# Kernel tuning notes

Hardware: AMD Instinct MI355X
Metric: run time of the kernel (lower is better)

## Reference

```python
import jax, jax.numpy as jnp
import numpy as np

B, C, L, OUT = 64, 256, 4096, 256
EPS = 1e-5


def setup_inputs() -> dict:
    key = jax.random.key(0)
    ks = jax.random.split(key, 8)
    s = 1.0 / np.sqrt(C)
    return {
        "x": jax.random.normal(ks[0], (B, C, L), dtype=jnp.float32),
        "Wq": jax.random.normal(ks[1], (C, C), dtype=jnp.float32) * s,
        "Wk": jax.random.normal(ks[2], (C, C), dtype=jnp.float32) * s,
        "Wv": jax.random.normal(ks[3], (C, C), dtype=jnp.float32) * s,
        "Wc": jax.random.normal(ks[4], (C, C), dtype=jnp.float32) * s,
        "Wout": jax.random.normal(ks[5], (OUT, C), dtype=jnp.float32) * s,
        "gamma": jnp.ones((C,), dtype=jnp.float32),
        "beta": jnp.zeros((C,), dtype=jnp.float32),
    }


def _conv1x1(W, x):
    # 1x1 Conv1d, no bias: (O,C) x (B,C,L) -> (B,O,L)
    return jnp.einsum("oc,bcl->bol", W, x)


def reference(x, Wq, Wk, Wv, Wc, Wout, gamma, beta):
    q = _conv1x1(Wq, x)  # (B,C,L)
    k = _conv1x1(Wk, x)  # (B,C,L)
    v = _conv1x1(Wv, x)  # (B,C,L)
    # batch-wise attention: att[b,d,l] = sum_c q[b,c,l]*k[d,c,l] / sqrt(C)
    att = jnp.einsum("bcl,dcl->bdl", q, k) / jnp.sqrt(jnp.asarray(C, x.dtype))
    att = jax.nn.softmax(att, axis=1)  # softmax over the key-batch axis
    # virt[b,c,l] = sum_d att[b,d,l] * v[d,c,l]
    virt = jnp.einsum("bdl,dcl->bcl", att, v)
    # GroupNorm(1, C): normalize over (C,L) per sample, per-channel affine
    mean = jnp.mean(virt, axis=(1, 2), keepdims=True)
    var = jnp.var(virt, axis=(1, 2), keepdims=True)
    virt = (virt - mean) * jax.lax.rsqrt(var + EPS)
    virt = virt * gamma[None, :, None] + beta[None, :, None]
    virt = jax.nn.relu(virt)
    virt = _conv1x1(Wc, virt)
    # dropout is identity in eval mode
    y = x + virt
    return _conv1x1(Wout, y)
```

## Files before the change

kernel.cpp:

```cpp
#include <hip/hip_runtime.h>


typedef __attribute__((ext_vector_type(8))) short          v8s;
typedef __attribute__((ext_vector_type(8))) unsigned short v8u;
typedef __attribute__((ext_vector_type(4))) unsigned short v4u;
typedef __attribute__((ext_vector_type(4))) float          f32x4;

#define MFMA16(a, b, c) __builtin_amdgcn_mfma_f32_16x16x32_bf16((a), (b), (c), 0, 0, 0)

#define GLOAD16(g, l)                                                            \
  __builtin_amdgcn_global_load_lds(                                              \
      (const __attribute__((address_space(1))) unsigned int*)(const void*)(g),   \
      (__attribute__((address_space(3))) unsigned int*)(void*)(l), 16, 0, 0)

static __device__ __forceinline__ unsigned short f2bf(float f) {
  union { float f; unsigned u; } v; v.f = f;
  unsigned r = (v.u + 0x7FFFu + ((v.u >> 16) & 1u)) >> 16;
  return (unsigned short)r;
}
static __device__ __forceinline__ float bf2f(unsigned short h) {
  union { unsigned u; float f; } v; v.u = ((unsigned)h) << 16; return v.f;
}

__global__ void k_prep(const float* __restrict__ Wq, const float* __restrict__ Wk,
                       const float* __restrict__ Wv, const float* __restrict__ Wc,
                       const float* __restrict__ Wout,
                       unsigned short* __restrict__ Wtv,
                       unsigned short* __restrict__ Wout2,
                       float* __restrict__ stats) {
  int bid = blockIdx.x, j = threadIdx.x;
  if (bid < 256) {
    int i = bid;
    float acc = 0.f;
    for (int c = 0; c < 256; ++c) acc += Wq[c * 256 + i] * Wk[c * 256 + j];
    Wtv[i * 256 + j] = f2bf(acc * 0.0625f);
    Wtv[(256 + i) * 256 + j] = f2bf(Wv[i * 256 + j]);
  } else if (bid < 512) {
    int o = bid - 256;
    float acc = 0.f;
    for (int c = 0; c < 256; ++c) acc += Wout[o * 256 + c] * Wc[c * 256 + j];
    Wout2[o * 512 + 256 + j] = f2bf(acc);
    Wout2[o * 512 + j] = f2bf(Wout[o * 256 + j]);
  } else {
    stats[(bid - 512) * 256 + j] = 0.f;
  }
}

__global__ void k_transpose(const float* __restrict__ x, unsigned short* __restrict__ Xt) {
  __shared__ float tile[64 * 65];
  int bid = blockIdx.x;
  int b = bid >> 8, cb = (bid >> 6) & 3, lb = bid & 63;
  int c0 = cb * 64, l0 = lb * 64, t = threadIdx.x;
#pragma unroll
  for (int i = 0; i < 4; ++i) {
    int idx = i * 256 + t, r = idx >> 4, ch = idx & 15;
    float4 v = *(const float4*)(x + ((size_t)(b * 256 + c0 + r)) * 4096 + l0 + ch * 4);
    tile[r * 65 + ch * 4 + 0] = v.x; tile[r * 65 + ch * 4 + 1] = v.y;
    tile[r * 65 + ch * 4 + 2] = v.z; tile[r * 65 + ch * 4 + 3] = v.w;
  }
  __syncthreads();
#pragma unroll
  for (int i = 0; i < 2; ++i) {
    int idx = i * 256 + t, r = idx >> 3, ch = idx & 7;
    v8u o;
#pragma unroll
    for (int j = 0; j < 8; ++j) o[j] = f2bf(tile[(ch * 8 + j) * 65 + r]);
    *(v8u*)(Xt + ((size_t)(b * 4096 + l0 + r)) * 256 + c0 + ch * 8) = o;
  }
}

__global__ __launch_bounds__(512, 4) void k_fused(const unsigned short* __restrict__ Xt,
                                                  const unsigned short* __restrict__ Wtv,
                                                  unsigned short* __restrict__ Virt,
                                                  float* __restrict__ stats) {
  extern __shared__ char smem[];
  unsigned short* Xs  = (unsigned short*)(smem);
  unsigned short* Tb  = (unsigned short*)(smem + 33792);
  unsigned short* Ps  = (unsigned short*)(smem + 70656);
  float*          red = (float*)(smem + 79872);
  float*          rowv= (float*)(smem + 80896);

  int l = blockIdx.x, t = threadIdx.x, lane = t & 63, w = t >> 6;
  int fr = lane & 15, kq = (lane >> 4) * 8, qr = (lane >> 4) * 4;

#pragma unroll
  for (int i = 0; i < 4; ++i) {
    int idx = i * 512 + t, r = idx >> 5, ch = idx & 31;
    *(v8u*)(Xs + r * 264 + ch * 8) = *(const v8u*)(Xt + ((size_t)(r * 4096 + l)) * 256 + ch * 8);
  }
  __syncthreads();

  {
    int n0 = w * 32;
    f32x4 acc[4][2];
#pragma unroll
    for (int mi = 0; mi < 4; ++mi)
#pragma unroll
      for (int nj = 0; nj < 2; ++nj) acc[mi][nj] = (f32x4){0.f, 0.f, 0.f, 0.f};
#pragma unroll
    for (int kc = 0; kc < 8; ++kc) {
      v8s a[4], b[2];
#pragma unroll
      for (int mi = 0; mi < 4; ++mi) a[mi] = *(const v8s*)(Xs + (mi * 16 + fr) * 264 + kc * 32 + kq);
#pragma unroll
      for (int nj = 0; nj < 2; ++nj)
        b[nj] = *(const v8s*)(Wtv + ((size_t)(n0 + nj * 16 + fr)) * 256 + kc * 32 + kq);
#pragma unroll
      for (int mi = 0; mi < 4; ++mi)
#pragma unroll
        for (int nj = 0; nj < 2; ++nj) acc[mi][nj] = MFMA16(a[mi], b[nj], acc[mi][nj]);
    }
#pragma unroll
    for (int mi = 0; mi < 4; ++mi)
#pragma unroll
      for (int nj = 0; nj < 2; ++nj)
#pragma unroll
        for (int i = 0; i < 4; ++i)
          Tb[(mi * 16 + qr + i) * 264 + n0 + nj * 16 + fr] = f2bf(acc[mi][nj][i]);
  }
  __syncthreads();

  int b0 = (w & 3) * 16, dp = (w >> 2) * 2, half = w >> 2;
  f32x4 sacc[2];
  sacc[0] = (f32x4){0.f, 0.f, 0.f, 0.f};
  sacc[1] = (f32x4){0.f, 0.f, 0.f, 0.f};
  {
#pragma unroll
    for (int kc = 0; kc < 8; ++kc) {
      v8s bb = *(const v8s*)(Xs + (b0 + fr) * 264 + kc * 32 + kq);
#pragma unroll
      for (int j = 0; j < 2; ++j) {
        v8s a = *(const v8s*)(Tb + ((dp + j) * 16 + fr) * 264 + kc * 32 + kq);
        sacc[j] = MFMA16(a, bb, sacc[j]);
      }
    }
    float pm = -1e30f;
#pragma unroll
    for (int j = 0; j < 2; ++j)
#pragma unroll
      for (int i = 0; i < 4; ++i) pm = fmaxf(pm, sacc[j][i]);
    pm = fmaxf(pm, __shfl_xor(pm, 16));
    pm = fmaxf(pm, __shfl_xor(pm, 32));
    if (lane < 16) red[(b0 + lane) * 4 + half] = pm;
  }
  __syncthreads();

  {
    float m = fmaxf(red[(b0 + fr) * 4 + 0], red[(b0 + fr) * 4 + 1]);
    float ps = 0.f;
#pragma unroll
    for (int j = 0; j < 2; ++j) {
      v4u pk;
#pragma unroll
      for (int i = 0; i < 4; ++i) {
        float e = __expf(sacc[j][i] - m);
        ps += e;
        pk[i] = f2bf(e);
      }
      *(v4u*)(Ps + (b0 + fr) * 72 + (dp + j) * 16 + qr) = pk;
    }
    ps += __shfl_xor(ps, 16);
    ps += __shfl_xor(ps, 32);
    if (lane < 16) red[(b0 + lane) * 4 + 2 + half] = ps;
  }

  {
    int c0 = w * 32;
    f32x4 vacc[2][4];
#pragma unroll
    for (int ci = 0; ci < 2; ++ci)
#pragma unroll
      for (int di = 0; di < 4; ++di) vacc[ci][di] = (f32x4){0.f, 0.f, 0.f, 0.f};
#pragma unroll
    for (int kc = 0; kc < 8; ++kc) {
      v8s a[2], b[4];
#pragma unroll
      for (int ci = 0; ci < 2; ++ci)
        a[ci] = *(const v8s*)(Wtv + ((size_t)(256 + c0 + ci * 16 + fr)) * 256 + kc * 32 + kq);
#pragma unroll
      for (int di = 0; di < 4; ++di) b[di] = *(const v8s*)(Xs + (di * 16 + fr) * 264 + kc * 32 + kq);
#pragma unroll
      for (int ci = 0; ci < 2; ++ci)
#pragma unroll
        for (int di = 0; di < 4; ++di) vacc[ci][di] = MFMA16(a[ci], b[di], vacc[ci][di]);
    }
#pragma unroll
    for (int ci = 0; ci < 2; ++ci)
#pragma unroll
      for (int di = 0; di < 4; ++di)
#pragma unroll
        for (int i = 0; i < 4; ++i)
          Tb[(c0 + ci * 16 + qr + i) * 72 + di * 16 + fr] = f2bf(vacc[ci][di][i]);
  }
  __syncthreads();

  if (t < 64) rowv[t] = 1.f / (red[t * 4 + 2] + red[t * 4 + 3]);

  f32x4 pacc[4][2];
#pragma unroll
  for (int mi = 0; mi < 4; ++mi) { pacc[mi][0] = (f32x4){0,0,0,0}; pacc[mi][1] = (f32x4){0,0,0,0}; }
  {
    int n0 = w * 32;
#pragma unroll
    for (int kc = 0; kc < 2; ++kc) {
      v8s a[4], b[2];
#pragma unroll
      for (int mi = 0; mi < 4; ++mi) a[mi] = *(const v8s*)(Ps + (mi * 16 + fr) * 72 + kc * 32 + kq);
#pragma unroll
      for (int nj = 0; nj < 2; ++nj)
        b[nj] = *(const v8s*)(Tb + (n0 + nj * 16 + fr) * 72 + kc * 32 + kq);
#pragma unroll
      for (int mi = 0; mi < 4; ++mi)
#pragma unroll
        for (int nj = 0; nj < 2; ++nj) pacc[mi][nj] = MFMA16(a[mi], b[nj], pacc[mi][nj]);
    }
  }
  __syncthreads();

  {
    int n0 = w * 32;
#pragma unroll
    for (int mi = 0; mi < 4; ++mi)
#pragma unroll
      for (int i = 0; i < 4; ++i) {
        float inv = rowv[mi * 16 + qr + i];
#pragma unroll
        for (int nj = 0; nj < 2; ++nj)
          Tb[(mi * 16 + qr + i) * 264 + n0 + nj * 16 + fr] = f2bf(pacc[mi][nj][i] * inv);
      }
  }
  __syncthreads();

  {
    int r = t >> 3, seg = t & 7;
    float s = 0.f, s2 = 0.f;
#pragma unroll
    for (int c4 = 0; c4 < 4; ++c4) {
      v8u v = *(const v8u*)(Tb + r * 264 + seg * 32 + c4 * 8);
#pragma unroll
      for (int j = 0; j < 8; ++j) { float f = bf2f(v[j]); s += f; s2 += f * f; }
      *(v8u*)(Virt + ((size_t)(r * 4096 + l)) * 256 + seg * 32 + c4 * 8) = v;
    }
#pragma unroll
    for (int o = 4; o > 0; o >>= 1) { s += __shfl_xor(s, o); s2 += __shfl_xor(s2, o); }
    if (seg == 0) {
      int slot = blockIdx.x & 31;
      atomicAdd(&stats[slot * 128 + r], s);
      atomicAdd(&stats[slot * 128 + 64 + r], s2);
    }
  }
}

__global__ void k_finalize(float* __restrict__ stats) {
  int t = threadIdx.x;
  if (t < 64) {
    float s = 0.f, s2 = 0.f;
    for (int sl = 0; sl < 32; ++sl) { s += stats[sl * 128 + t]; s2 += stats[sl * 128 + 64 + t]; }
    const float inv = 1.f / 1048576.f;
    float m = s * inv;
    float var = s2 * inv - m * m;
    stats[4096 + t] = m;
    stats[4160 + t] = rsqrtf(var + 1e-5f);
  }
}

__global__ __launch_bounds__(512, 2) void k_gemm_out(const unsigned short* __restrict__ Xt,
                                                     const unsigned short* __restrict__ Virt,
                                                     const unsigned short* __restrict__ Wout2,
                                                     const float* __restrict__ stats,
                                                     const float* __restrict__ gamma,
                                                     const float* __restrict__ beta,
                                                     float* __restrict__ out) {
  extern __shared__ char smem[];
  int t = threadIdx.x, lane = t & 63, w = t >> 6;
  int fr = lane & 15;
  int wm = w >> 2, wn = w & 3;
  size_t t0 = (size_t)blockIdx.x * 256;
  int b = (int)(t0 >> 12);
  float mean = stats[4096 + b], rstd = stats[4160 + b];

  f32x4 acc[8][4];
#pragma unroll
  for (int mi = 0; mi < 8; ++mi)
#pragma unroll
    for (int ni = 0; ni < 4; ++ni) acc[mi][ni] = (f32x4){0.f, 0.f, 0.f, 0.f};

  int srow = (lane >> 3);
  int sph = lane & 7;

#define STAGE_TILE(BUF, KC)                                                          \
  do {                                                                               \
    char* base_ = smem + (BUF) * 65536;                                              \
    if (w < 4) {                                                                     \
      const unsigned short* s0_ =                                                    \
          ((KC) < 4) ? (Xt + (KC) * 64) : (Virt + ((KC) - 4) * 64);                  \
      _Pragma("unroll") for (int g_ = 0; g_ < 8; ++g_) {                             \
        int r_ = w * 64 + g_ * 8 + srow;                                             \
        int sl_ = sph ^ (r_ & 7);                                                    \
        GLOAD16(s0_ + (t0 + r_) * 256 + sl_ * 8, base_ + w * 8192 + g_ * 1024);      \
      }                                                                              \
    } else {                                                                         \
      int wb_ = w - 4;                                                               \
      _Pragma("unroll") for (int g_ = 0; g_ < 8; ++g_) {                             \
        int r_ = wb_ * 64 + g_ * 8 + srow;                                           \
        int sl_ = sph ^ (r_ & 7);                                                    \
        GLOAD16(Wout2 + r_ * 512 + (KC) * 64 + sl_ * 8,                              \
                base_ + 32768 + wb_ * 8192 + g_ * 1024);                             \
      }                                                                              \
    }                                                                                \
  } while (0)

  STAGE_TILE(0, 0);
  __syncthreads();

  for (int kc = 0; kc < 8; ++kc) {
    int cur = kc & 1;
    if (kc < 7) STAGE_TILE(cur ^ 1, kc + 1);

    {
      const char* Ab = smem + cur * 65536;
      const char* Bb = Ab + 32768;
#pragma unroll
      for (int ks = 0; ks < 2; ++ks) {
        int xr = (ks * 64 + (lane >> 4) * 16) ^ ((fr & 7) << 4);
        v8s a[8], bb[4];
#pragma unroll
        for (int mi = 0; mi < 8; ++mi)
          a[mi] = *(const v8s*)(Ab + (wm * 128 + mi * 16 + fr) * 128 + xr);
#pragma unroll
        for (int ni = 0; ni < 4; ++ni)
          bb[ni] = *(const v8s*)(Bb + (wn * 64 + ni * 16 + fr) * 128 + xr);
#pragma unroll
        for (int mi = 0; mi < 8; ++mi)
#pragma unroll
          for (int ni = 0; ni < 4; ++ni) acc[mi][ni] = MFMA16(a[mi], bb[ni], acc[mi][ni]);
      }
    }
    __syncthreads();

    if (kc < 7 && kc >= 3) {
      char* Ab = smem + (cur ^ 1) * 65536;
      int s_log = sph ^ ((t >> 3) & 7);
      int cb = (kc + 1 - 4) * 64 + s_log * 8;
      float4 g0 = *(const float4*)(gamma + cb), g1 = *(const float4*)(gamma + cb + 4);
      float4 b0 = *(const float4*)(beta + cb), b1 = *(const float4*)(beta + cb + 4);
      float rg[8] = {g0.x * rstd, g0.y * rstd, g0.z * rstd, g0.w * rstd,
                     g1.x * rstd, g1.y * rstd, g1.z * rstd, g1.w * rstd};
      float sh[8] = {b0.x - mean * rg[0], b0.y - mean * rg[1], b0.z - mean * rg[2],
                     b0.w - mean * rg[3], b1.x - mean * rg[4], b1.y - mean * rg[5],
                     b1.z - mean * rg[6], b1.w - mean * rg[7]};
#pragma unroll
      for (int j = 0; j < 4; ++j) {
        int r = j * 64 + (t >> 3);
        v8u* p = (v8u*)(Ab + r * 128 + sph * 16);
        v8u v = *p, o;
#pragma unroll
        for (int e = 0; e < 8; ++e) {
          float z = fmaf(bf2f(v[e]), rg[e], sh[e]);
          o[e] = f2bf(fmaxf(z, 0.f));
        }
        *p = o;
      }
      __syncthreads();
    }
  }
#undef STAGE_TILE

  int qr = (lane >> 4) * 4, lbase = (int)(t0 & 4095);
#pragma unroll
  for (int mi = 0; mi < 8; ++mi)
#pragma unroll
    for (int ni = 0; ni < 4; ++ni)
#pragma unroll
      for (int i = 0; i < 4; ++i) {
        int ll = lbase + wm * 128 + mi * 16 + qr + i;
        int o = wn * 64 + ni * 16 + fr;
        out[((size_t)(b * 256 + o)) * 4096 + ll] = acc[mi][ni][i];
      }
}

extern "C" void kernel_launch(void* const* d_in, const int* in_sizes, int n_in,
                              void* d_out, int out_size, void* d_ws, size_t ws_size,
                              hipStream_t stream) {
  const float* x     = (const float*)d_in[0];
  const float* Wq    = (const float*)d_in[1];
  const float* Wk    = (const float*)d_in[2];
  const float* Wv    = (const float*)d_in[3];
  const float* Wc    = (const float*)d_in[4];
  const float* Wout  = (const float*)d_in[5];
  const float* gamma = (const float*)d_in[6];
  const float* beta  = (const float*)d_in[7];
  float* out = (float*)d_out;
  char* ws = (char*)d_ws;
  unsigned short* Xt   = (unsigned short*)(ws);
  unsigned short* Virt = (unsigned short*)(ws + 134217728ull);
  unsigned short* Wtv  = (unsigned short*)(ws + 268435456ull);
  unsigned short* W2   = (unsigned short*)(ws + 268697600ull);
  float* stats         = (float*)(ws + 268959744ull);

  static const int kFusedLds = 81152;
  static const int kGemmLds  = 131072;
  hipFuncSetAttribute((const void*)k_fused, hipFuncAttributeMaxDynamicSharedMemorySize,
                      kFusedLds);
  hipFuncSetAttribute((const void*)k_gemm_out, hipFuncAttributeMaxDynamicSharedMemorySize,
                      kGemmLds);

  k_prep<<<528, 256, 0, stream>>>(Wq, Wk, Wv, Wc, Wout, Wtv, W2, stats);
  k_transpose<<<16384, 256, 0, stream>>>(x, Xt);
  k_fused<<<4096, 512, kFusedLds, stream>>>(Xt, Wtv, Virt, stats);
  k_finalize<<<1, 64, 0, stream>>>(stats);
  k_gemm_out<<<1024, 512, kGemmLds, stream>>>(Xt, Virt, W2, stats, gamma, beta, out);
}
```

Baseline: 797.9 us.

## Process two positions per block with prefetch, 32x32 MFMA, swizzled LDS

The fused attention kernel now handles two sequence positions per block (the grid is halved) and prefetches the next position's X tile into registers while the current one computes. The projection and PV GEMMs switch from 16x16x32 to 32x32x16 MFMA tiles, and the X tile in LDS uses an XOR-swizzled layout with no padding, aimed at avoiding bank conflicts. s_setprio hints are placed around the MFMA loops. This is meant to hide global load latency and cut per-block overhead, at the cost of higher register pressure and fewer blocks to spread across CUs.

```diff
diff --git a/kernel.cpp b/kernel.cpp
--- a/kernel.cpp
+++ b/kernel.cpp
@@ -5,8 +5,10 @@
 typedef __attribute__((ext_vector_type(8))) unsigned short v8u;
 typedef __attribute__((ext_vector_type(4))) unsigned short v4u;
 typedef __attribute__((ext_vector_type(4))) float          f32x4;
+typedef __attribute__((ext_vector_type(16))) float         f32x16;
 
 #define MFMA16(a, b, c) __builtin_amdgcn_mfma_f32_16x16x32_bf16((a), (b), (c), 0, 0, 0)
+#define MFMA32(a, b, c) __builtin_amdgcn_mfma_f32_32x32x16_bf16((a), (b), (c), 0, 0, 0)
 
 #define GLOAD16(g, l)                                                            \
   __builtin_amdgcn_global_load_lds(                                              \
@@ -20,6 +22,12 @@
 }
 static __device__ __forceinline__ float bf2f(unsigned short h) {
   union { unsigned u; float f; } v; v.u = ((unsigned)h) << 16; return v.f;
+}
+static __device__ __forceinline__ f32x16 z16() {
+  f32x16 z;
+#pragma unroll
+  for (int i = 0; i < 16; ++i) z[i] = 0.f;
+  return z;
 }
 
 __global__ void k_prep(const float* __restrict__ Wq, const float* __restrict__ Wk,
@@ -74,181 +82,186 @@
                                                   unsigned short* __restrict__ Virt,
                                                   float* __restrict__ stats) {
   extern __shared__ char smem[];
-  unsigned short* Xs  = (unsigned short*)(smem);
-  unsigned short* Tb  = (unsigned short*)(smem + 33792);
-  unsigned short* Ps  = (unsigned short*)(smem + 70656);
-  float*          red = (float*)(smem + 79872);
-  float*          rowv= (float*)(smem + 80896);
-
-  int l = blockIdx.x, t = threadIdx.x, lane = t & 63, w = t >> 6;
+  unsigned short* Tb  = (unsigned short*)(smem + 32768);
+  unsigned short* Ps  = (unsigned short*)(smem + 69632);
+  float*          red = (float*)(smem + 78848);
+  float*          rowv= (float*)(smem + 79872);
+
+  int t = threadIdx.x, lane = t & 63, w = t >> 6;
   int fr = lane & 15, kq = (lane >> 4) * 8, qr = (lane >> 4) * 4;
-
+  int c32 = lane & 31, kh = lane >> 5;
+
+#define XS_PTR(row, chunk) (smem + (((row)) << 9) + ((((chunk) << 4)) ^ (((row) & 31) << 4)))
+
+  {
+    int l0 = blockIdx.x;
+#pragma unroll
+    for (int i = 0; i < 4; ++i) {
+      int idx = i * 512 + t, r = idx >> 5, ch = idx & 31;
+      v8u v = *(const v8u*)(Xt + ((size_t)(r * 4096 + l0)) * 256 + ch * 8);
+      *(v8u*)XS_PTR(r, ch) = v;
+    }
+  }
+  __syncthreads();
+
+  v8u xn[4];
 #pragma unroll
   for (int i = 0; i < 4; ++i) {
     int idx = i * 512 + t, r = idx >> 5, ch = idx & 31;
-    *(v8u*)(Xs + r * 264 + ch * 8) = *(const v8u*)(Xt + ((size_t)(r * 4096 + l)) * 256 + ch * 8);
-  }
-  __syncthreads();
-
-  {
-    int n0 = w * 32;
-    f32x4 acc[4][2];
-#pragma unroll
-    for (int mi = 0; mi < 4; ++mi)
-#pragma unroll
-      for (int nj = 0; nj < 2; ++nj) acc[mi][nj] = (f32x4){0.f, 0.f, 0.f, 0.f};
-#pragma unroll
-    for (int kc = 0; kc < 8; ++kc) {
-      v8s a[4], b[2];
-#pragma unroll
-      for (int mi = 0; mi < 4; ++mi) a[mi] = *(const v8s*)(Xs + (mi * 16 + fr) * 264 + kc * 32 + kq);
-#pragma unroll
-      for (int nj = 0; nj < 2; ++nj)
-        b[nj] = *(const v8s*)(Wtv + ((size_t)(n0 + nj * 16 + fr)) * 256 + kc * 32 + kq);
-#pragma unroll
-      for (int mi = 0; mi < 4; ++mi)
-#pragma unroll
-        for (int nj = 0; nj < 2; ++nj) acc[mi][nj] = MFMA16(a[mi], b[nj], acc[mi][nj]);
-    }
-#pragma unroll
-    for (int mi = 0; mi < 4; ++mi)
-#pragma unroll
-      for (int nj = 0; nj < 2; ++nj)
-#pragma unroll
-        for (int i = 0; i < 4; ++i)
-          Tb[(mi * 16 + qr + i) * 264 + n0 + nj * 16 + fr] = f2bf(acc[mi][nj][i]);
-  }
-  __syncthreads();
-
-  int b0 = (w & 3) * 16, dp = (w >> 2) * 2, half = w >> 2;
-  f32x4 sacc[2];
-  sacc[0] = (f32x4){0.f, 0.f, 0.f, 0.f};
-  sacc[1] = (f32x4){0.f, 0.f, 0.f, 0.f};
-  {
-#pragma unroll
-    for (int kc = 0; kc < 8; ++kc) {
-      v8s bb = *(const v8s*)(Xs + (b0 + fr) * 264 + kc * 32 + kq);
+    xn[i] = *(const v8u*)(Xt + ((size_t)(r * 4096 + blockIdx.x + 2048)) * 256 + ch * 8);
+  }
+
+#pragma unroll 1
+  for (int it = 0; it < 2; ++it) {
+    int l = blockIdx.x + it * 2048;
+
+    {
+      int n0 = w * 32;
+      f32x16 acc0 = z16(), acc1 = z16();
+      __builtin_amdgcn_s_setprio(1);
+#pragma unroll
+      for (int ks = 0; ks < 16; ++ks) {
+        v8s a0 = *(const v8s*)XS_PTR(c32, ks * 2 + kh);
+        v8s a1 = *(const v8s*)XS_PTR(32 + c32, ks * 2 + kh);
+        v8s b = *(const v8s*)(Wtv + ((size_t)(n0 + c32)) * 256 + ks * 16 + kh * 8);
+        acc0 = MFMA32(a0, b, acc0);
+        acc1 = MFMA32(a1, b, acc1);
+      }
+      __builtin_amdgcn_s_setprio(0);
+#pragma unroll
+      for (int reg = 0; reg < 16; ++reg) {
+        int rr = (reg & 3) + 8 * (reg >> 2) + 4 * kh;
+        Tb[rr * 264 + n0 + c32] = f2bf(acc0[reg]);
+        Tb[(32 + rr) * 264 + n0 + c32] = f2bf(acc1[reg]);
+      }
+    }
+    __syncthreads();
+
+    int b0 = (w & 3) * 16, dp = (w >> 2) * 2, hv = w >> 2;
+    f32x4 sacc[2];
+    sacc[0] = (f32x4){0.f, 0.f, 0.f, 0.f};
+    sacc[1] = (f32x4){0.f, 0.f, 0.f, 0.f};
+    {
+      __builtin_amdgcn_s_setprio(1);
+#pragma unroll
+      for (int kc = 0; kc < 8; ++kc) {
+        v8s bb = *(const v8s*)XS_PTR(b0 + fr, kc * 4 + (lane >> 4));
+#pragma unroll
+        for (int j = 0; j < 2; ++j) {
+          v8s a = *(const v8s*)(Tb + ((dp + j) * 16 + fr) * 264 + kc * 32 + kq);
+          sacc[j] = MFMA16(a, bb, sacc[j]);
+        }
+      }
+      __builtin_amdgcn_s_setprio(0);
+      float pm = -1e30f;
+#pragma unroll
+      for (int j = 0; j < 2; ++j)
+#pragma unroll
+        for (int i = 0; i < 4; ++i) pm = fmaxf(pm, sacc[j][i]);
+      pm = fmaxf(pm, __shfl_xor(pm, 16));
+      pm = fmaxf(pm, __shfl_xor(pm, 32));
+      if (lane < 16) red[(b0 + lane) * 4 + hv] = pm;
+    }
+    __syncthreads();
+
+    {
+      float m = fmaxf(red[(b0 + fr) * 4 + 0], red[(b0 + fr) * 4 + 1]);
+      float ps = 0.f;
 #pragma unroll
       for (int j = 0; j < 2; ++j) {
-        v8s a = *(const v8s*)(Tb + ((dp + j) * 16 + fr) * 264 + kc * 32 + kq);
-        sacc[j] = MFMA16(a, bb, sacc[j]);
-      }
-    }
-    float pm = -1e30f;
-#pragma unroll
-    for (int j = 0; j < 2; ++j)
-#pragma unroll
-      for (int i = 0; i < 4; ++i) pm = fmaxf(pm, sacc[j][i]);
-    pm = fmaxf(pm, __shfl_xor(pm, 16));
-    pm = fmaxf(pm, __shfl_xor(pm, 32));
-    if (lane < 16) red[(b0 + lane) * 4 + half] = pm;
-  }
-  __syncthreads();
-
-  {
-    float m = fmaxf(red[(b0 + fr) * 4 + 0], red[(b0 + fr) * 4 + 1]);
-    float ps = 0.f;
-#pragma unroll
-    for (int j = 0; j < 2; ++j) {
-      v4u pk;
+        v4u pk;
+#pragma unroll
+        for (int i = 0; i < 4; ++i) {
+          float e = __expf(sacc[j][i] - m);
+          ps += e;
+          pk[i] = f2bf(e);
+        }
+        *(v4u*)(Ps + (b0 + fr) * 72 + (dp + j) * 16 + qr) = pk;
+      }
+      ps += __shfl_xor(ps, 16);
+      ps += __shfl_xor(ps, 32);
+      if (lane < 16) red[(b0 + lane) * 4 + 2 + hv] = ps;
+    }
+
+    {
+      int c0 = w * 32;
+      f32x16 vacc0 = z16(), vacc1 = z16();
+      __builtin_amdgcn_s_setprio(1);
+#pragma unroll
+      for (int ks = 0; ks < 16; ++ks) {
+        v8s a = *(const v8s*)(Wtv + ((size_t)(256 + c0 + c32)) * 256 + ks * 16 + kh * 8);
+        v8s b0v = *(const v8s*)XS_PTR(c32, ks * 2 + kh);
+        v8s b1v = *(const v8s*)XS_PTR(32 + c32, ks * 2 + kh);
+        vacc0 = MFMA32(a, b0v, vacc0);
+        vacc1 = MFMA32(a, b1v, vacc1);
+      }
+      __builtin_amdgcn_s_setprio(0);
+#pragma unroll
+      for (int reg = 0; reg < 16; ++reg) {
+        int rr = (reg & 3) + 8 * (reg >> 2) + 4 * kh;
+        Tb[(c0 + rr) * 72 + c32] = f2bf(vacc0[reg]);
+        Tb[(c0 + rr) * 72 + 32 + c32] = f2bf(vacc1[reg]);
+      }
+    }
+    __syncthreads();
+
+    if (t < 64) rowv[t] = 1.f / (red[t * 4 + 2] + red[t * 4 + 3]);
+
+    f32x16 pacc0 = z16(), pacc1 = z16();
+    {
+      int n0 = w * 32;
+      __builtin_amdgcn_s_setprio(1);
+#pragma unroll
+      for (int ks = 0; ks < 4; ++ks) {
+        v8s a0 = *(const v8s*)(Ps + c32 * 72 + ks * 16 + kh * 8);
+        v8s a1 = *(const v8s*)(Ps + (32 + c32) * 72 + ks * 16 + kh * 8);
+        v8s bv = *(const v8s*)(Tb + (n0 + c32) * 72 + ks * 16 + kh * 8);
+        pacc0 = MFMA32(a0, bv, pacc0);
+        pacc1 = MFMA32(a1, bv, pacc1);
+      }
+      __builtin_amdgcn_s_setprio(0);
+    }
+    if (it == 0) {
 #pragma unroll
       for (int i = 0; i < 4; ++i) {
-        float e = __expf(sacc[j][i] - m);
-        ps += e;
-        pk[i] = f2bf(e);
-      }
-      *(v4u*)(Ps + (b0 + fr) * 72 + (dp + j) * 16 + qr) = pk;
-    }
-    ps += __shfl_xor(ps, 16);
-    ps += __shfl_xor(ps, 32);
-    if (lane < 16) red[(b0 + lane) * 4 + 2 + half] = ps;
-  }
-
-  {
-    int c0 = w * 32;
-    f32x4 vacc[2][4];
-#pragma unroll
-    for (int ci = 0; ci < 2; ++ci)
-#pragma unroll
-      for (int di = 0; di < 4; ++di) vacc[ci][di] = (f32x4){0.f, 0.f, 0.f, 0.f};
-#pragma unroll
-    for (int kc = 0; kc < 8; ++kc) {
-      v8s a[2], b[4];
-#pragma unroll
-      for (int ci = 0; ci < 2; ++ci)
-        a[ci] = *(const v8s*)(Wtv + ((size_t)(256 + c0 + ci * 16 + fr)) * 256 + kc * 32 + kq);
-#pragma unroll
-      for (int di = 0; di < 4; ++di) b[di] = *(const v8s*)(Xs + (di * 16 + fr) * 264 + kc * 32 + kq);
-#pragma unroll
-      for (int ci = 0; ci < 2; ++ci)
-#pragma unroll
-        for (int di = 0; di < 4; ++di) vacc[ci][di] = MFMA16(a[ci], b[di], vacc[ci][di]);
-    }
-#pragma unroll
-    for (int ci = 0; ci < 2; ++ci)
-#pragma unroll
-      for (int di = 0; di < 4; ++di)
-#pragma unroll
-        for (int i = 0; i < 4; ++i)
-          Tb[(c0 + ci * 16 + qr + i) * 72 + di * 16 + fr] = f2bf(vacc[ci][di][i]);
-  }
-  __syncthreads();
-
-  if (t < 64) rowv[t] = 1.f / (red[t * 4 + 2] + red[t * 4 + 3]);
-
-  f32x4 pacc[4][2];
-#pragma unroll
-  for (int mi = 0; mi < 4; ++mi) { pacc[mi][0] = (f32x4){0,0,0,0}; pacc[mi][1] = (f32x4){0,0,0,0}; }
-  {
-    int n0 = w * 32;
-#pragma unroll
-    for (int kc = 0; kc < 2; ++kc) {
-      v8s a[4], b[2];
-#pragma unroll
-      for (int mi = 0; mi < 4; ++mi) a[mi] = *(const v8s*)(Ps + (mi * 16 + fr) * 72 + kc * 32 + kq);
-#pragma unroll
-      for (int nj = 0; nj < 2; ++nj)
-        b[nj] = *(const v8s*)(Tb + (n0 + nj * 16 + fr) * 72 + kc * 32 + kq);
-#pragma unroll
-      for (int mi = 0; mi < 4; ++mi)
-#pragma unroll
-        for (int nj = 0; nj < 2; ++nj) pacc[mi][nj] = MFMA16(a[mi], b[nj], pacc[mi][nj]);
-    }
-  }
-  __syncthreads();
-
-  {
-    int n0 = w * 32;
-#pragma unroll
-    for (int mi = 0; mi < 4; ++mi)
-#pragma unroll
-      for (int i = 0; i < 4; ++i) {
-        float inv = rowv[mi * 16 + qr + i];
-#pragma unroll
-        for (int nj = 0; nj < 2; ++nj)
-          Tb[(mi * 16 + qr + i) * 264 + n0 + nj * 16 + fr] = f2bf(pacc[mi][nj][i] * inv);
-      }
-  }
-  __syncthreads();
-
-  {
-    int r = t >> 3, seg = t & 7;
-    float s = 0.f, s2 = 0.f;
-#pragma unroll
-    for (int c4 = 0; c4 < 4; ++c4) {
-      v8u v = *(const v8u*)(Tb + r * 264 + seg * 32 + c4 * 8);
-#pragma unroll
-      for (int j = 0; j < 8; ++j) { float f = bf2f(v[j]); s += f; s2 += f * f; }
-      *(v8u*)(Virt + ((size_t)(r * 4096 + l)) * 256 + seg * 32 + c4 * 8) = v;
-    }
-#pragma unroll
-    for (int o = 4; o > 0; o >>= 1) { s += __shfl_xor(s, o); s2 += __shfl_xor(s2, o); }
-    if (seg == 0) {
-      int slot = blockIdx.x & 31;
-      atomicAdd(&stats[slot * 128 + r], s);
-      atomicAdd(&stats[slot * 128 + 64 + r], s2);
-    }
-  }
+        int idx = i * 512 + t, r = idx >> 5, ch = idx & 31;
+        *(v8u*)XS_PTR(r, ch) = xn[i];
+      }
+    }
+    __syncthreads();
+
+    {
+      int n0 = w * 32;
+#pragma unroll
+      for (int reg = 0; reg < 16; ++reg) {
+        int rr = (reg & 3) + 8 * (reg >> 2) + 4 * kh;
+        Tb[rr * 264 + n0 + c32] = f2bf(pacc0[reg] * rowv[rr]);
+        Tb[(32 + rr) * 264 + n0 + c32] = f2bf(pacc1[reg] * rowv[32 + rr]);
+      }
+    }
+    __syncthreads();
+
+    {
+      int r = t >> 3, seg = t & 7;
+      float s = 0.f, s2 = 0.f;
+#pragma unroll
+      for (int c4 = 0; c4 < 4; ++c4) {
+        v8u v = *(const v8u*)(Tb + r * 264 + seg * 32 + c4 * 8);
+#pragma unroll
+        for (int j = 0; j < 8; ++j) { float f = bf2f(v[j]); s += f; s2 += f * f; }
+        *(v8u*)(Virt + ((size_t)(r * 4096 + l)) * 256 + seg * 32 + c4 * 8) = v;
+      }
+#pragma unroll
+      for (int o = 4; o > 0; o >>= 1) { s += __shfl_xor(s, o); s2 += __shfl_xor(s2, o); }
+      if (seg == 0) {
+        int slot = blockIdx.x & 31;
+        atomicAdd(&stats[slot * 128 + r], s);
+        atomicAdd(&stats[slot * 128 + 64 + r], s2);
+      }
+    }
+    if (it == 0) __syncthreads();
+  }
+#undef XS_PTR
 }
 
 __global__ void k_finalize(float* __restrict__ stats) {
@@ -398,7 +411,7 @@
   unsigned short* W2   = (unsigned short*)(ws + 268697600ull);
   float* stats         = (float*)(ws + 268959744ull);
 
-  static const int kFusedLds = 81152;
+  static const int kFusedLds = 80128;
   static const int kGemmLds  = 131072;
   hipFuncSetAttribute((const void*)k_fused, hipFuncAttributeMaxDynamicSharedMemorySize,
                       kFusedLds);
@@ -407,7 +420,7 @@
 
   k_prep<<<528, 256, 0, stream>>>(Wq, Wk, Wv, Wc, Wout, Wtv, W2, stats);
   k_transpose<<<16384, 256, 0, stream>>>(x, Xt);
-  k_fused<<<4096, 512, kFusedLds, stream>>>(Xt, Wtv, Virt, stats);
+  k_fused<<<2048, 512, kFusedLds, stream>>>(Xt, Wtv, Virt, stats);
   k_finalize<<<1, 64, 0, stream>>>(stats);
   k_gemm_out<<<1024, 512, kGemmLds, stream>>>(Xt, Virt, W2, stats, gamma, beta, out);
 }
```

Result: slower. 1.061 ms (+33.0%).
